# Performance work log

Hardware: AMD Instinct MI355X
Metric: run time of the kernel (lower is better)

## Reference

```python
import jax, jax.numpy as jnp
import numpy as np

BLANK_ID = 0


def setup_inputs() -> dict:
    key = jax.random.key(0)
    ks = jax.random.split(key, 8)
    B, T, H, V = 32, 1000, 640, 5000
    s = 0.02
    tn_output = jax.random.normal(ks[0], (B, T, H), dtype=jnp.float32)
    embed = jax.random.normal(ks[1], (V, H), dtype=jnp.float32) * s
    Wx = jax.random.normal(ks[2], (H, 4 * H), dtype=jnp.float32) * s  # LSTM input weights
    Wh = jax.random.normal(ks[3], (H, 4 * H), dtype=jnp.float32) * s  # LSTM recurrent weights
    b = jnp.zeros((4 * H,), dtype=jnp.float32)
    Wc = jax.random.normal(ks[4], (H, V), dtype=jnp.float32) * s     # classifier weights
    bc = jnp.zeros((V,), dtype=jnp.float32)
    return {"tn_output": tn_output, "embed": embed, "Wx": Wx, "Wh": Wh,
            "b": b, "Wc": Wc, "bc": bc}


def _lstm_step(tok, h, c, embed, Wx, Wh, b):
    # tok: [B] int32, h/c: [B,H]
    x = embed[tok]                                   # [B,H] gather (PN embedding)
    g = x @ Wx + h @ Wh + b                          # [B,4H]
    i, f, gg, o = jnp.split(g, 4, axis=-1)
    c2 = jax.nn.sigmoid(f) * c + jax.nn.sigmoid(i) * jnp.tanh(gg)
    h2 = jax.nn.sigmoid(o) * jnp.tanh(c2)
    return h2, c2


def reference(tn_output, embed, Wx, Wh, b, Wc, bc):
    """Batched transducer greedy decode (beam_size=1 path).
    Per t: joint = tanh(TN_t + out_PN); logits = joint @ Wc + bc; log_softmax;
    argmax; if != blank, emit token, accumulate logp, advance PN state (masked).
    Returns (logp_scores [B], predictions [B,T] with blank where no emission).
    """
    B, T, H = tn_output.shape
    tok0 = jnp.full((B,), BLANK_ID, dtype=jnp.int32)
    h0 = jnp.zeros((B, H), dtype=tn_output.dtype)
    c0 = jnp.zeros((B, H), dtype=tn_output.dtype)
    # initial PN forward on the blank token (hidden = None -> zeros)
    h, c = _lstm_step(tok0, h0, c0, embed, Wx, Wh, b)
    out_PN = h

    def step(carry, tn_t):
        h, c, out_PN, tok, scores = carry
        logits = jnp.tanh(tn_t + out_PN) @ Wc + bc            # joint ('sum') + classifier
        logp = jax.nn.log_softmax(logits, axis=-1)            # [B,V]
        pos = jnp.argmax(logp, axis=-1)                       # [B]
        val = jnp.max(logp, axis=-1)                          # [B]
        upd = pos != BLANK_ID
        scores = scores + jnp.where(upd, val, 0.0)
        new_tok = jnp.where(upd, pos.astype(jnp.int32), tok)
        h2, c2 = _lstm_step(new_tok, h, c, embed, Wx, Wh, b)
        m = upd[:, None]
        h = jnp.where(m, h2, h)
        c = jnp.where(m, c2, c)
        out_PN = jnp.where(m, h2, out_PN)
        emit = jnp.where(upd, pos, BLANK_ID).astype(jnp.int32)
        return (h, c, out_PN, new_tok, scores), emit

    carry0 = (h, c, out_PN, tok0, jnp.zeros((B,), dtype=tn_output.dtype))
    (h, c, out_PN, tok, scores), emits = jax.lax.scan(
        step, carry0, jnp.swapaxes(tn_output, 0, 1))          # scan over time
    preds = jnp.swapaxes(emits, 0, 1)                          # [B,T]
    return scores, preds
```

## Files before the change

### kernel.cpp

```cpp
#include <hip/hip_runtime.h>
#include <float.h>

#define BB 32
#define TT 1000
#define HH 640
#define H4 2560
#define VV 5000
#define NLOG 157
#define NGATE 80
#define NB   240

#define O_JOINT 0
#define O_HT    20480
#define O_PM    40960
#define O_PS    46080
#define O_PI    51200
#define O_BAR   56320
#define O_CT    56960
#define O_PNT   77440
#define O_XWXB  97920
#define XWXB_ELEMS ((size_t)VV * (size_t)H4)
#define O_WHP   (O_XWXB + 12800000)
#define WHP_ELEMS ((size_t)NGATE * HH * 32)

typedef unsigned int u32;
typedef unsigned long long u64;
typedef float vf4 __attribute__((ext_vector_type(4)));

__device__ __forceinline__ float sigf(float x) { return 1.0f / (1.0f + expf(-x)); }

__device__ __forceinline__ float ldc1(const float* p) {
  u32 v = __hip_atomic_load((const u32*)p, __ATOMIC_RELAXED, __HIP_MEMORY_SCOPE_AGENT);
  return __uint_as_float(v);
}
__device__ __forceinline__ void stc1(float* p, float x) {
  __hip_atomic_store((u32*)p, __float_as_uint(x), __ATOMIC_RELAXED, __HIP_MEMORY_SCOPE_AGENT);
}

__device__ __forceinline__ void stage_sc1_full(float* dst, const float* src, int tid) {
  const float* p0 = src + 4 * (tid + 0 * 512);
  const float* p1 = src + 4 * (tid + 1 * 512);
  const float* p2 = src + 4 * (tid + 2 * 512);
  const float* p3 = src + 4 * (tid + 3 * 512);
  const float* p4 = src + 4 * (tid + 4 * 512);
  const float* p5 = src + 4 * (tid + 5 * 512);
  const float* p6 = src + 4 * (tid + 6 * 512);
  const float* p7 = src + 4 * (tid + 7 * 512);
  const float* p8 = src + 4 * (tid + 8 * 512);
  const float* p9 = src + 4 * (tid + 9 * 512);
  float4 a0, a1, a2, a3, a4, a5, a6, a7, a8, a9;
  asm volatile(
      "global_load_dwordx4 %0, %10, off sc0 sc1\n\t"
      "global_load_dwordx4 %1, %11, off sc0 sc1\n\t"
      "global_load_dwordx4 %2, %12, off sc0 sc1\n\t"
      "global_load_dwordx4 %3, %13, off sc0 sc1\n\t"
      "global_load_dwordx4 %4, %14, off sc0 sc1\n\t"
      "global_load_dwordx4 %5, %15, off sc0 sc1\n\t"
      "global_load_dwordx4 %6, %16, off sc0 sc1\n\t"
      "global_load_dwordx4 %7, %17, off sc0 sc1\n\t"
      "global_load_dwordx4 %8, %18, off sc0 sc1\n\t"
      "global_load_dwordx4 %9, %19, off sc0 sc1\n\t"
      "s_waitcnt vmcnt(0)"
      : "=&v"(a0), "=&v"(a1), "=&v"(a2), "=&v"(a3), "=&v"(a4),
        "=&v"(a5), "=&v"(a6), "=&v"(a7), "=&v"(a8), "=&v"(a9)
      : "v"(p0), "v"(p1), "v"(p2), "v"(p3), "v"(p4),
        "v"(p5), "v"(p6), "v"(p7), "v"(p8), "v"(p9)
      : "memory");
  float4* d4 = (float4*)dst;
  d4[tid + 0 * 512] = a0;
  d4[tid + 1 * 512] = a1;
  d4[tid + 2 * 512] = a2;
  d4[tid + 3 * 512] = a3;
  d4[tid + 4 * 512] = a4;
  d4[tid + 5 * 512] = a5;
  d4[tid + 6 * 512] = a6;
  d4[tid + 7 * 512] = a7;
  d4[tid + 8 * 512] = a8;
  d4[tid + 9 * 512] = a9;
}

__device__ __forceinline__ void grid_bar(unsigned* bar, unsigned epoch) {
  __syncthreads();
  if (threadIdx.x == 0) {
    const int g = (int)blockIdx.x / 30;
    unsigned* cnt = bar + g * 32;
    unsigned* gen = bar + (9 + g) * 32;
    asm volatile("s_waitcnt vmcnt(0)" ::: "memory");
    unsigned a = __hip_atomic_fetch_add(cnt, 1u, __ATOMIC_RELAXED, __HIP_MEMORY_SCOPE_AGENT);
    if (a == 30u * epoch - 1u) {
      unsigned* root = bar + 8 * 32;
      unsigned r = __hip_atomic_fetch_add(root, 1u, __ATOMIC_RELAXED, __HIP_MEMORY_SCOPE_AGENT);
      if (r == 8u * epoch - 1u) {
#pragma unroll
        for (int i = 0; i < 8; ++i)
          __hip_atomic_store(bar + (9 + i) * 32, epoch, __ATOMIC_RELAXED, __HIP_MEMORY_SCOPE_AGENT);
      }
    }
    while (__hip_atomic_load(gen, __ATOMIC_RELAXED, __HIP_MEMORY_SCOPE_AGENT) < epoch)
      __builtin_amdgcn_s_sleep(1);
  }
  __syncthreads();
}

__global__ __launch_bounds__(256) void precompute_k(const float* __restrict__ embed,
                                                    const float* __restrict__ Wx,
                                                    const float* __restrict__ bias,
                                                    float* __restrict__ xwxb) {
  __shared__ float embT[HH * 17];
  const int tid = threadIdx.x;
  const int v0 = blockIdx.y * 16;
  const int c0 = blockIdx.x * 256 + (tid & 63) * 4;
  const int vg = tid >> 6;
  for (int i = tid; i < 16 * 160; i += 256) {
    int vr = i / 160, kq = i - vr * 160;
    int v = v0 + vr; if (v >= VV) v = VV - 1;
    float4 e = *(const float4*)&embed[(size_t)v * HH + kq * 4];
    embT[(kq * 4 + 0) * 17 + vr] = e.x;
    embT[(kq * 4 + 1) * 17 + vr] = e.y;
    embT[(kq * 4 + 2) * 17 + vr] = e.z;
    embT[(kq * 4 + 3) * 17 + vr] = e.w;
  }
  __syncthreads();
  float acc[16];
#pragma unroll
  for (int i = 0; i < 16; ++i) acc[i] = 0.f;
#pragma unroll 4
  for (int k = 0; k < HH; ++k) {
    float4 wv = *(const float4*)&Wx[(size_t)k * H4 + c0];
#pragma unroll
    for (int i = 0; i < 4; ++i) {
      float e = embT[k * 17 + vg * 4 + i];
      acc[i * 4 + 0] += e * wv.x;
      acc[i * 4 + 1] += e * wv.y;
      acc[i * 4 + 2] += e * wv.z;
      acc[i * 4 + 3] += e * wv.w;
    }
  }
  float4 bv = *(const float4*)&bias[c0];
#pragma unroll
  for (int i = 0; i < 4; ++i) {
    int v = v0 + vg * 4 + i;
    if (v < VV) {
      float4 r;
      r.x = acc[i * 4 + 0] + bv.x; r.y = acc[i * 4 + 1] + bv.y;
      r.z = acc[i * 4 + 2] + bv.z; r.w = acc[i * 4 + 3] + bv.w;
      *(float4*)&xwxb[(size_t)v * H4 + c0] = r;
    }
  }
}

__global__ __launch_bounds__(256) void repack_k(const float* __restrict__ Wh,
                                                float* __restrict__ whp) {
  const int q = blockIdx.x;
  for (int i = threadIdx.x; i < HH * 32; i += 256) {
    int k = i >> 5, lc = i & 31;
    whp[((size_t)q * HH + k) * 32 + lc] =
        Wh[(size_t)k * H4 + (lc >> 3) * HH + q * 8 + (lc & 7)];
  }
}

__global__ __launch_bounds__(256) void init_k(const float* __restrict__ tn,
                                              const float* __restrict__ embed,
                                              const float* __restrict__ Wx,
                                              const float* __restrict__ bias,
                                              float* ws, int use_table) {
  const int tid = threadIdx.x, bid = blockIdx.x;
  const int b = tid & 31, c8 = tid >> 5;
  const int j = bid * 8 + c8;
  if (bid == 0) {
    unsigned* bar = (unsigned*)(ws + O_BAR);
    for (int i = tid; i < 17 * 32; i += 256) bar[i] = 0u;
  }
  const float* xwxb = ws + O_XWXB;
  float g4[4];
  if (use_table) {
#pragma unroll
    for (int g = 0; g < 4; ++g) g4[g] = xwxb[g * HH + j];
  } else {
#pragma unroll
    for (int g = 0; g < 4; ++g) g4[g] = bias[g * HH + j];
#pragma unroll 4
    for (int k = 0; k < HH; ++k) {
      float xv = embed[k];
#pragma unroll
      for (int g = 0; g < 4; ++g) g4[g] += xv * Wx[(size_t)k * H4 + g * HH + j];
    }
  }
  float c1 = sigf(g4[0]) * tanhf(g4[2]);
  float h1 = sigf(g4[3]) * tanhf(c1);
  ws[O_CT + j * 32 + b] = c1;
  ws[O_HT + j * 32 + b] = h1;
  ws[O_PNT + j * 32 + b] = h1;
  ws[O_JOINT + j * 32 + b] = tanhf(tn[(size_t)b * TT * HH + j] + h1);
}

__global__ __launch_bounds__(512) void decode_k(const float* __restrict__ tn,
                                                const float* __restrict__ embed,
                                                const float* __restrict__ Wx,
                                                const float* __restrict__ bias,
                                                const float* __restrict__ Wh,
                                                const float* __restrict__ Wc,
                                                const float* __restrict__ bc,
                                                float* __restrict__ out,
                                                float* ws, int use_table, int use_pack) {
  __shared__ float joint_s[20480];
  __shared__ float smem[10800];
  __shared__ float hwh_s[1056];
  __shared__ float c_s[256];
  __shared__ float pn_s[256];
  __shared__ int s_tok[32];
  __shared__ int s_upd[32];
  __shared__ int s_ptok[32];
  __shared__ float s_scores[32];
  const int tid = threadIdx.x, bid = blockIdx.x;
  unsigned* bar = (unsigned*)(ws + O_BAR);
  const float* xwxb = ws + O_XWXB;
  const bool is_log = (bid < NLOG);
  const bool is_gate = (bid >= NLOG) && (bid < NLOG + NGATE);
  const int q = bid - NLOG;

  if (tid < 32) { s_ptok[tid] = 0; s_scores[tid] = 0.f; }
  if (is_gate && tid < 256) {
    const int jj = tid >> 5, b = tid & 31;
    c_s[jj * 32 + b] = ws[O_CT + (q * 8 + jj) * 32 + b];
    pn_s[jj * 32 + b] = ws[O_PNT + (q * 8 + jj) * 32 + b];
  }
  __syncthreads();

  const int lane = tid & 63, wvv = tid >> 6;
  const int sub = lane >> 5;
  const int cg  = lane & 3;
  const int bg  = (lane >> 2) & 7;
  const int kb  = (wvv * 2 + sub) * 40;
  const float* wbase;
  int wstride;
  if (is_log) {
    int c = bid * 32 + cg * 8;
    if (c > VV - 8) c = VV - 8;
    wbase = Wc + (size_t)kb * VV + c;
    wstride = VV;
  } else if (use_pack) {
    wbase = ws + O_WHP + ((size_t)q * HH + kb) * 32 + cg * 8;
    wstride = 32;
  } else {
    wbase = Wh + (size_t)kb * H4 + cg * HH + q * 8;
    wstride = H4;
  }
  const float* jb0 = joint_s + kb * 32 + bg * 4;

  unsigned epoch = 0;
  for (int t = 0; t < TT; ++t) {
    float tnv = 0.f;

    if (is_log || is_gate) {
      if (is_gate && tid < 256 && t + 1 < TT)
        tnv = tn[((size_t)(tid & 31) * TT + (t + 1)) * HH + q * 8 + (tid >> 5)];
      stage_sc1_full(joint_s, ws + (is_log ? O_JOINT : O_HT), tid);
      __syncthreads();

      float acc[32];
#pragma unroll
      for (int i = 0; i < 32; ++i) acc[i] = 0.f;
      if (is_log) {
        const float* wp = wbase;
        const float* jp = jb0;
#pragma unroll 4
        for (int kk = 0; kk < 40; ++kk) {
          float4 w0 = *(const float4*)(wp);
          float4 w1 = *(const float4*)(wp + 4);
          float4 jv = *(const float4*)(jp);
          wp += wstride;
          jp += 32;
          acc[0]  += w0.x * jv.x; acc[1]  += w0.x * jv.y; acc[2]  += w0.x * jv.z; acc[3]  += w0.x * jv.w;
          acc[4]  += w0.y * jv.x; acc[5]  += w0.y * jv.y; acc[6]  += w0.y * jv.z; acc[7]  += w0.y * jv.w;
          acc[8]  += w0.z * jv.x; acc[9]  += w0.z * jv.y; acc[10] += w0.z * jv.z; acc[11] += w0.z * jv.w;
          acc[12] += w0.w * jv.x; acc[13] += w0.w * jv.y; acc[14] += w0.w * jv.z; acc[15] += w0.w * jv.w;
          acc[16] += w1.x * jv.x; acc[17] += w1.x * jv.y; acc[18] += w1.x * jv.z; acc[19] += w1.x * jv.w;
          acc[20] += w1.y * jv.x; acc[21] += w1.y * jv.y; acc[22] += w1.y * jv.z; acc[23] += w1.y * jv.w;
          acc[24] += w1.z * jv.x; acc[25] += w1.z * jv.y; acc[26] += w1.z * jv.z; acc[27] += w1.z * jv.w;
          acc[28] += w1.w * jv.x; acc[29] += w1.w * jv.y; acc[30] += w1.w * jv.z; acc[31] += w1.w * jv.w;
        }
      } else {
        const float* wp = wbase;
        const float* jp = jb0;
#pragma unroll 4
        for (int kk = 0; kk < 40; ++kk) {
          vf4 w0 = __builtin_nontemporal_load((const vf4*)(wp));
          vf4 w1 = __builtin_nontemporal_load((const vf4*)(wp + 4));
          float4 jv = *(const float4*)(jp);
          wp += wstride;
          jp += 32;
          acc[0]  += w0.x * jv.x; acc[1]  += w0.x * jv.y; acc[2]  += w0.x * jv.z; acc[3]  += w0.x * jv.w;
          acc[4]  += w0.y * jv.x; acc[5]  += w0.y * jv.y; acc[6]  += w0.y * jv.z; acc[7]  += w0.y * jv.w;
          acc[8]  += w0.z * jv.x; acc[9]  += w0.z * jv.y; acc[10] += w0.z * jv.z; acc[11] += w0.z * jv.w;
          acc[12] += w0.w * jv.x; acc[13] += w0.w * jv.y; acc[14] += w0.w * jv.z; acc[15] += w0.w * jv.w;
          acc[16] += w1.x * jv.x; acc[17] += w1.x * jv.y; acc[18] += w1.x * jv.z; acc[19] += w1.x * jv.w;
          acc[20] += w1.y * jv.x; acc[21] += w1.y * jv.y; acc[22] += w1.y * jv.z; acc[23] += w1.y * jv.w;
          acc[24] += w1.z * jv.x; acc[25] += w1.z * jv.y; acc[26] += w1.z * jv.z; acc[27] += w1.z * jv.w;
          acc[28] += w1.w * jv.x; acc[29] += w1.w * jv.y; acc[30] += w1.w * jv.z; acc[31] += w1.w * jv.w;
        }
      }
#pragma unroll
      for (int i = 0; i < 32; ++i) acc[i] += __shfl_xor(acc[i], 32);
      float* part = smem;
      if (sub == 0) {
        float* pb = part + wvv * 1152 + bg * 4;
#pragma unroll
        for (int c = 0; c < 8; ++c)
          *(float4*)&pb[(cg * 8 + c) * 36] =
              make_float4(acc[c * 4 + 0], acc[c * 4 + 1], acc[c * 4 + 2], acc[c * 4 + 3]);
      }
      __syncthreads();

      const int b = tid & 31, colg = tid >> 5;
      if (is_log) {
        float* lm = smem + 9216;
        float* lsv = smem + 9744;
        int* lix = (int*)(smem + 10272);
        float m = -FLT_MAX; int ix = 0;
        float lv[2];
#pragma unroll
        for (int i = 0; i < 2; ++i) {
          const int cl = colg * 2 + i;
          float s = 0.f;
#pragma unroll
          for (int qq = 0; qq < 8; ++qq) s += part[qq * 1152 + cl * 36 + b];
          int cgl = bid * 32 + cl;
          float l = (cgl < VV) ? s + bc[cgl] : -FLT_MAX;
          lv[i] = l;
          if (l > m) { m = l; ix = cgl; }
        }
        float e = 0.f;
        if (m > -FLT_MAX) {
#pragma unroll
          for (int i = 0; i < 2; ++i) e += expf(lv[i] - m);
        }
        lm[colg * 33 + b] = m; lsv[colg * 33 + b] = e; lix[colg * 33 + b] = ix;
        __syncthreads();
        if (tid < 32) {
          float m2 = lm[tid], s2 = lsv[tid]; int ix2 = lix[tid];
#pragma unroll
          for (int qq = 1; qq < 16; ++qq) {
            float M = lm[qq * 33 + tid], S = lsv[qq * 33 + tid]; int I = lix[qq * 33 + tid];
            if (M > m2) { s2 = s2 * expf(m2 - M) + S; m2 = M; ix2 = I; }
            else if (M > -FLT_MAX) { s2 += S * expf(M - m2); }
          }
          stc1(&ws[O_PM + bid * 32 + tid], m2);
          stc1(&ws[O_PS + bid * 32 + tid], s2);
          stc1(&ws[O_PI + bid * 32 + tid], __int_as_float(ix2));
        }
      } else {
#pragma unroll
        for (int i = 0; i < 2; ++i) {
          const int cl = colg * 2 + i;
          float s = 0.f;
#pragma unroll
          for (int qq = 0; qq < 8; ++qq) s += part[qq * 1152 + cl * 36 + b];
          hwh_s[cl * 33 + b] = s;
        }
      }
    }
    epoch++;
    grid_bar(bar, epoch);

    if (is_gate) {
      float* rm = smem;
      float* rs = smem + 528;
      int* ri = (int*)(smem + 1056);
      float* gmat = smem + 1584;
      float* xl = smem + 2640;
      const int r = tid & 31, c16 = tid >> 5;
      {
        float Ms[10], Ss[10]; int Is[10];
#pragma unroll
        for (int i = 0; i < 10; ++i) {
          int idx = c16 * 10 + i;
          bool v = (idx < NLOG);
          int ic = v ? idx : 0;
          Ms[i] = ldc1(&ws[O_PM + ic * 32 + r]);
          Ss[i] = ldc1(&ws[O_PS + ic * 32 + r]);
          Is[i] = __float_as_int(ldc1(&ws[O_PI + ic * 32 + r]));
          if (!v) { Ms[i] = -FLT_MAX; Ss[i] = 0.f; Is[i] = 0; }
        }
        float m = -FLT_MAX, s = 0.f; int ix = 0;
#pragma unroll
        for (int i = 0; i < 10; ++i) {
          if (Ms[i] > m) { s = s * expf(m - Ms[i]) + Ss[i]; m = Ms[i]; ix = Is[i]; }
          else if (Ms[i] > -FLT_MAX) { s += Ss[i] * expf(Ms[i] - m); }
        }
        rm[c16 * 33 + r] = m; rs[c16 * 33 + r] = s; ri[c16 * 33 + r] = ix;
      }
      __syncthreads();
      if (tid < 32) {
        float m = rm[tid], s = rs[tid]; int ix = ri[tid];
#pragma unroll
        for (int qq = 1; qq < 16; ++qq) {
          float M = rm[qq * 33 + tid], S = rs[qq * 33 + tid]; int I = ri[qq * 33 + tid];
          if (M > m) { s = s * expf(m - M) + S; m = M; ix = I; }
          else { s += S * expf(M - m); }
        }
        int pos = ix;
        int upd = (pos != 0) ? 1 : 0;
        int ntk = upd ? pos : s_ptok[tid];
        s_tok[tid] = ntk; s_upd[tid] = upd; s_ptok[tid] = ntk;
        if (bid == NLOG) {
          float sc = s_scores[tid];
          if (upd) sc -= logf(s);
          s_scores[tid] = sc;
          out[BB + (size_t)tid * TT + t] = upd ? (float)pos : 0.0f;
          if (t == TT - 1) out[tid] = sc;
        }
      }
      __syncthreads();

      const int b = tid & 31;
      float gv[2];
#pragma unroll
      for (int h = 0; h < 2; ++h) {
        int lc = (tid >> 5) + h * 16;
        int wcol = (lc >> 3) * HH + q * 8 + (lc & 7);
        float v = hwh_s[lc * 33 + b];
        if (use_table) v += __builtin_nontemporal_load(&xwxb[(size_t)s_tok[b] * H4 + wcol]);
        else v += bias[wcol];
        gv[h] = v;
      }
      if (!use_table) {
        for (int st = 0; st < 4; ++st) {
          const int k0 = st * 160;
          __syncthreads();
          for (int i = tid; i < 32 * 160; i += 512) {
            int bb = i / 160, kk = i - bb * 160;
            xl[bb * 161 + kk] = embed[(size_t)s_tok[bb] * HH + k0 + kk];
          }
          __syncthreads();
          for (int k = 0; k < 160; ++k) {
            float xv = xl[b * 161 + k];
#pragma unroll
            for (int h = 0; h < 2; ++h) {
              int lc = (tid >> 5) + h * 16;
              int wcol = (lc >> 3) * HH + q * 8 + (lc & 7);
              gv[h] += xv * Wx[(size_t)(k0 + k) * H4 + wcol];
            }
          }
        }
      }
#pragma unroll
      for (int h = 0; h < 2; ++h) {
        int lc = (tid >> 5) + h * 16;
        gmat[lc * 33 + b] = gv[h];
      }
      __syncthreads();
      if (tid < 256) {
        const int jj = tid >> 5, b2 = tid & 31;
        float gi = gmat[(0 * 8 + jj) * 33 + b2];
        float gf = gmat[(1 * 8 + jj) * 33 + b2];
        float gg = gmat[(2 * 8 + jj) * 33 + b2];
        float go = gmat[(3 * 8 + jj) * 33 + b2];
        float cold = c_s[jj * 32 + b2];
        float c2 = sigf(gf) * cold + sigf(gi) * tanhf(gg);
        float h2 = sigf(go) * tanhf(c2);
        float pv;
        if (s_upd[b2]) {
          c_s[jj * 32 + b2] = c2;
          pn_s[jj * 32 + b2] = h2;
          stc1(&ws[O_HT + (q * 8 + jj) * 32 + b2], h2);
          pv = h2;
        } else {
          pv = pn_s[jj * 32 + b2];
        }
        if (t + 1 < TT)
          stc1(&ws[O_JOINT + (q * 8 + jj) * 32 + b2], tanhf(tnv + pv));
      }
    }
    epoch++;
    grid_bar(bar, epoch);
  }
}

extern "C" void kernel_launch(void* const* d_in, const int* in_sizes, int n_in,
                              void* d_out, int out_size, void* d_ws, size_t ws_size,
                              hipStream_t stream) {
  const float* tn    = (const float*)d_in[0];
  const float* embed = (const float*)d_in[1];
  const float* Wx    = (const float*)d_in[2];
  const float* Wh    = (const float*)d_in[3];
  const float* bias  = (const float*)d_in[4];
  const float* Wc    = (const float*)d_in[5];
  const float* bc    = (const float*)d_in[6];
  float* out = (float*)d_out;
  float* ws  = (float*)d_ws;

  const size_t need_table = (size_t)(O_XWXB + XWXB_ELEMS) * sizeof(float);
  const size_t need_pack  = (size_t)(O_WHP + WHP_ELEMS) * sizeof(float);
  const int use_table = (ws_size >= need_table) ? 1 : 0;
  const int use_pack  = (ws_size >= need_pack) ? 1 : 0;

  if (use_table)
    hipLaunchKernelGGL(precompute_k, dim3(10, 313), dim3(256), 0, stream,
                       embed, Wx, bias, ws + O_XWXB);
  if (use_pack)
    hipLaunchKernelGGL(repack_k, dim3(NGATE), dim3(256), 0, stream, Wh, ws + O_WHP);
  hipLaunchKernelGGL(init_k, dim3(80), dim3(256), 0, stream, tn, embed, Wx, bias, ws, use_table);
  hipLaunchKernelGGL(decode_k, dim3(NB), dim3(512), 0, stream,
                     tn, embed, Wx, bias, Wh, Wc, bc, out, ws, use_table, use_pack);
}
```

Baseline: 19.06 ms.

## Replace two grid barriers per step with point-to-point flag synchronization

Removes the hierarchical grid-wide barrier that ran twice per timestep. Logit blocks now publish a per-block progress flag, and gate blocks publish their own flag plus increment a counter once they have staged the previous hidden state. Gate blocks wait only on the flags they depend on, and the extra blocks exit early. This is meant to cut barrier latency and let the logit and gate phases overlap, at the cost of spin polling across many flags and more subtle memory-ordering requirements.

After: 30.97 ms. +62.5%, slower.

```diff
diff --git a/kernel.cpp b/kernel.cpp
--- a/kernel.cpp
+++ b/kernel.cpp
@@ -35,6 +35,12 @@
 }
 __device__ __forceinline__ void stc1(float* p, float x) {
   __hip_atomic_store((u32*)p, __float_as_uint(x), __ATOMIC_RELAXED, __HIP_MEMORY_SCOPE_AGENT);
+}
+__device__ __forceinline__ u32 ldu(const u32* p) {
+  return __hip_atomic_load(p, __ATOMIC_RELAXED, __HIP_MEMORY_SCOPE_AGENT);
+}
+__device__ __forceinline__ void stu(u32* p, u32 v) {
+  __hip_atomic_store(p, v, __ATOMIC_RELAXED, __HIP_MEMORY_SCOPE_AGENT);
 }
 
 __device__ __forceinline__ void stage_sc1_full(float* dst, const float* src, int tid) {
@@ -79,29 +85,6 @@
   d4[tid + 9 * 512] = a9;
 }
 
-__device__ __forceinline__ void grid_bar(unsigned* bar, unsigned epoch) {
-  __syncthreads();
-  if (threadIdx.x == 0) {
-    const int g = (int)blockIdx.x / 30;
-    unsigned* cnt = bar + g * 32;
-    unsigned* gen = bar + (9 + g) * 32;
-    asm volatile("s_waitcnt vmcnt(0)" ::: "memory");
-    unsigned a = __hip_atomic_fetch_add(cnt, 1u, __ATOMIC_RELAXED, __HIP_MEMORY_SCOPE_AGENT);
-    if (a == 30u * epoch - 1u) {
-      unsigned* root = bar + 8 * 32;
-      unsigned r = __hip_atomic_fetch_add(root, 1u, __ATOMIC_RELAXED, __HIP_MEMORY_SCOPE_AGENT);
-      if (r == 8u * epoch - 1u) {
-#pragma unroll
-        for (int i = 0; i < 8; ++i)
-          __hip_atomic_store(bar + (9 + i) * 32, epoch, __ATOMIC_RELAXED, __HIP_MEMORY_SCOPE_AGENT);
-      }
-    }
-    while (__hip_atomic_load(gen, __ATOMIC_RELAXED, __HIP_MEMORY_SCOPE_AGENT) < epoch)
-      __builtin_amdgcn_s_sleep(1);
-  }
-  __syncthreads();
-}
-
 __global__ __launch_bounds__(256) void precompute_k(const float* __restrict__ embed,
                                                     const float* __restrict__ Wx,
                                                     const float* __restrict__ bias,
@@ -168,7 +151,7 @@
   const int b = tid & 31, c8 = tid >> 5;
   const int j = bid * 8 + c8;
   if (bid == 0) {
-    unsigned* bar = (unsigned*)(ws + O_BAR);
+    u32* bar = (u32*)(ws + O_BAR);
     for (int i = tid; i < 17 * 32; i += 256) bar[i] = 0u;
   }
   const float* xwxb = ws + O_XWXB;
@@ -213,10 +196,14 @@
   __shared__ int s_ptok[32];
   __shared__ float s_scores[32];
   const int tid = threadIdx.x, bid = blockIdx.x;
-  unsigned* bar = (unsigned*)(ws + O_BAR);
-  const float* xwxb = ws + O_XWXB;
   const bool is_log = (bid < NLOG);
   const bool is_gate = (bid >= NLOG) && (bid < NLOG + NGATE);
+  if (!is_log && !is_gate) return;
+
+  u32* F1  = (u32*)(ws + O_BAR);
+  u32* F2  = (u32*)(ws + O_BAR) + 192;
+  u32* CRD = (u32*)(ws + O_BAR) + 288;
+  const float* xwxb = ws + O_XWXB;
   const int q = bid - NLOG;
 
   if (tid < 32) { s_ptok[tid] = 0; s_scores[tid] = 0.f; }
@@ -248,232 +235,249 @@
   }
   const float* jb0 = joint_s + kb * 32 + bg * 4;
 
-  unsigned epoch = 0;
   for (int t = 0; t < TT; ++t) {
+    if (tid < NGATE) {
+      while (ldu(F2 + tid) < (u32)t) __builtin_amdgcn_s_sleep(1);
+    }
+    __syncthreads();
+
     float tnv = 0.f;
-
-    if (is_log || is_gate) {
-      if (is_gate && tid < 256 && t + 1 < TT)
-        tnv = tn[((size_t)(tid & 31) * TT + (t + 1)) * HH + q * 8 + (tid >> 5)];
-      stage_sc1_full(joint_s, ws + (is_log ? O_JOINT : O_HT), tid);
+    if (is_gate && tid < 256 && t + 1 < TT)
+      tnv = tn[((size_t)(tid & 31) * TT + (t + 1)) * HH + q * 8 + (tid >> 5)];
+
+    stage_sc1_full(joint_s, ws + (is_log ? O_JOINT : O_HT), tid);
+    __syncthreads();
+    if (is_gate && tid == 0)
+      (void)__hip_atomic_fetch_add(CRD, 1u, __ATOMIC_RELAXED, __HIP_MEMORY_SCOPE_AGENT);
+
+    float acc[32];
+#pragma unroll
+    for (int i = 0; i < 32; ++i) acc[i] = 0.f;
+    if (is_log) {
+      const float* wp = wbase;
+      const float* jp = jb0;
+#pragma unroll 4
+      for (int kk = 0; kk < 40; ++kk) {
+        float4 w0 = *(const float4*)(wp);
+        float4 w1 = *(const float4*)(wp + 4);
+        float4 jv = *(const float4*)(jp);
+        wp += wstride;
+        jp += 32;
+        acc[0]  += w0.x * jv.x; acc[1]  += w0.x * jv.y; acc[2]  += w0.x * jv.z; acc[3]  += w0.x * jv.w;
+        acc[4]  += w0.y * jv.x; acc[5]  += w0.y * jv.y; acc[6]  += w0.y * jv.z; acc[7]  += w0.y * jv.w;
+        acc[8]  += w0.z * jv.x; acc[9]  += w0.z * jv.y; acc[10] += w0.z * jv.z; acc[11] += w0.z * jv.w;
+        acc[12] += w0.w * jv.x; acc[13] += w0.w * jv.y; acc[14] += w0.w * jv.z; acc[15] += w0.w * jv.w;
+        acc[16] += w1.x * jv.x; acc[17] += w1.x * jv.y; acc[18] += w1.x * jv.z; acc[19] += w1.x * jv.w;
+        acc[20] += w1.y * jv.x; acc[21] += w1.y * jv.y; acc[22] += w1.y * jv.z; acc[23] += w1.y * jv.w;
+        acc[24] += w1.z * jv.x; acc[25] += w1.z * jv.y; acc[26] += w1.z * jv.z; acc[27] += w1.z * jv.w;
+        acc[28] += w1.w * jv.x; acc[29] += w1.w * jv.y; acc[30] += w1.w * jv.z; acc[31] += w1.w * jv.w;
+      }
+    } else {
+      const float* wp = wbase;
+      const float* jp = jb0;
+#pragma unroll 4
+      for (int kk = 0; kk < 40; ++kk) {
+        vf4 w0 = __builtin_nontemporal_load((const vf4*)(wp));
+        vf4 w1 = __builtin_nontemporal_load((const vf4*)(wp + 4));
+        float4 jv = *(const float4*)(jp);
+        wp += wstride;
+        jp += 32;
+        acc[0]  += w0.x * jv.x; acc[1]  += w0.x * jv.y; acc[2]  += w0.x * jv.z; acc[3]  += w0.x * jv.w;
+        acc[4]  += w0.y * jv.x; acc[5]  += w0.y * jv.y; acc[6]  += w0.y * jv.z; acc[7]  += w0.y * jv.w;
+        acc[8]  += w0.z * jv.x; acc[9]  += w0.z * jv.y; acc[10] += w0.z * jv.z; acc[11] += w0.z * jv.w;
+        acc[12] += w0.w * jv.x; acc[13] += w0.w * jv.y; acc[14] += w0.w * jv.z; acc[15] += w0.w * jv.w;
+        acc[16] += w1.x * jv.x; acc[17] += w1.x * jv.y; acc[18] += w1.x * jv.z; acc[19] += w1.x * jv.w;
+        acc[20] += w1.y * jv.x; acc[21] += w1.y * jv.y; acc[22] += w1.y * jv.z; acc[23] += w1.y * jv.w;
+        acc[24] += w1.z * jv.x; acc[25] += w1.z * jv.y; acc[26] += w1.z * jv.z; acc[27] += w1.z * jv.w;
+        acc[28] += w1.w * jv.x; acc[29] += w1.w * jv.y; acc[30] += w1.w * jv.z; acc[31] += w1.w * jv.w;
+      }
+    }
+#pragma unroll
+    for (int i = 0; i < 32; ++i) acc[i] += __shfl_xor(acc[i], 32);
+    float* part = smem;
+    if (sub == 0) {
+      float* pb = part + wvv * 1152 + bg * 4;
+#pragma unroll
+      for (int c = 0; c < 8; ++c)
+        *(float4*)&pb[(cg * 8 + c) * 36] =
+            make_float4(acc[c * 4 + 0], acc[c * 4 + 1], acc[c * 4 + 2], acc[c * 4 + 3]);
+    }
+    __syncthreads();
+
+    const int b = tid & 31, colg = tid >> 5;
+    if (is_log) {
+      float* lm = smem + 9216;
+      float* lsv = smem + 9744;
+      int* lix = (int*)(smem + 10272);
+      float m = -FLT_MAX; int ix = 0;
+      float lv[2];
+#pragma unroll
+      for (int i = 0; i < 2; ++i) {
+        const int cl = colg * 2 + i;
+        float s = 0.f;
+#pragma unroll
+        for (int qq = 0; qq < 8; ++qq) s += part[qq * 1152 + cl * 36 + b];
+        int cgl = bid * 32 + cl;
+        float l = (cgl < VV) ? s + bc[cgl] : -FLT_MAX;
+        lv[i] = l;
+        if (l > m) { m = l; ix = cgl; }
+      }
+      float e = 0.f;
+      if (m > -FLT_MAX) {
+#pragma unroll
+        for (int i = 0; i < 2; ++i) e += expf(lv[i] - m);
+      }
+      lm[colg * 33 + b] = m; lsv[colg * 33 + b] = e; lix[colg * 33 + b] = ix;
       __syncthreads();
-
-      float acc[32];
-#pragma unroll
-      for (int i = 0; i < 32; ++i) acc[i] = 0.f;
-      if (is_log) {
-        const float* wp = wbase;
-        const float* jp = jb0;
-#pragma unroll 4
-        for (int kk = 0; kk < 40; ++kk) {
-          float4 w0 = *(const float4*)(wp);
-          float4 w1 = *(const float4*)(wp + 4);
-          float4 jv = *(const float4*)(jp);
-          wp += wstride;
-          jp += 32;
-          acc[0]  += w0.x * jv.x; acc[1]  += w0.x * jv.y; acc[2]  += w0.x * jv.z; acc[3]  += w0.x * jv.w;
-          acc[4]  += w0.y * jv.x; acc[5]  += w0.y * jv.y; acc[6]  += w0.y * jv.z; acc[7]  += w0.y * jv.w;
-          acc[8]  += w0.z * jv.x; acc[9]  += w0.z * jv.y; acc[10] += w0.z * jv.z; acc[11] += w0.z * jv.w;
-          acc[12] += w0.w * jv.x; acc[13] += w0.w * jv.y; acc[14] += w0.w * jv.z; acc[15] += w0.w * jv.w;
-          acc[16] += w1.x * jv.x; acc[17] += w1.x * jv.y; acc[18] += w1.x * jv.z; acc[19] += w1.x * jv.w;
-          acc[20] += w1.y * jv.x; acc[21] += w1.y * jv.y; acc[22] += w1.y * jv.z; acc[23] += w1.y * jv.w;
-          acc[24] += w1.z * jv.x; acc[25] += w1.z * jv.y; acc[26] += w1.z * jv.z; acc[27] += w1.z * jv.w;
-          acc[28] += w1.w * jv.x; acc[29] += w1.w * jv.y; acc[30] += w1.w * jv.z; acc[31] += w1.w * jv.w;
+      if (tid < 32) {
+        float m2 = lm[tid], s2 = lsv[tid]; int ix2 = lix[tid];
+#pragma unroll
+        for (int qq = 1; qq < 16; ++qq) {
+          float M = lm[qq * 33 + tid], S = lsv[qq * 33 + tid]; int I = lix[qq * 33 + tid];
+          if (M > m2) { s2 = s2 * expf(m2 - M) + S; m2 = M; ix2 = I; }
+          else if (M > -FLT_MAX) { s2 += S * expf(M - m2); }
         }
-      } else {
-        const float* wp = wbase;
-        const float* jp = jb0;
-#pragma unroll 4
-        for (int kk = 0; kk < 40; ++kk) {
-          vf4 w0 = __builtin_nontemporal_load((const vf4*)(wp));
-          vf4 w1 = __builtin_nontemporal_load((const vf4*)(wp + 4));
-          float4 jv = *(const float4*)(jp);
-          wp += wstride;
-          jp += 32;
-          acc[0]  += w0.x * jv.x; acc[1]  += w0.x * jv.y; acc[2]  += w0.x * jv.z; acc[3]  += w0.x * jv.w;
-          acc[4]  += w0.y * jv.x; acc[5]  += w0.y * jv.y; acc[6]  += w0.y * jv.z; acc[7]  += w0.y * jv.w;
-          acc[8]  += w0.z * jv.x; acc[9]  += w0.z * jv.y; acc[10] += w0.z * jv.z; acc[11] += w0.z * jv.w;
-          acc[12] += w0.w * jv.x; acc[13] += w0.w * jv.y; acc[14] += w0.w * jv.z; acc[15] += w0.w * jv.w;
-          acc[16] += w1.x * jv.x; acc[17] += w1.x * jv.y; acc[18] += w1.x * jv.z; acc[19] += w1.x * jv.w;
-          acc[20] += w1.y * jv.x; acc[21] += w1.y * jv.y; acc[22] += w1.y * jv.z; acc[23] += w1.y * jv.w;
-          acc[24] += w1.z * jv.x; acc[25] += w1.z * jv.y; acc[26] += w1.z * jv.z; acc[27] += w1.z * jv.w;
-          acc[28] += w1.w * jv.x; acc[29] += w1.w * jv.y; acc[30] += w1.w * jv.z; acc[31] += w1.w * jv.w;
-        }
-      }
-#pragma unroll
-      for (int i = 0; i < 32; ++i) acc[i] += __shfl_xor(acc[i], 32);
-      float* part = smem;
-      if (sub == 0) {
-        float* pb = part + wvv * 1152 + bg * 4;
-#pragma unroll
-        for (int c = 0; c < 8; ++c)
-          *(float4*)&pb[(cg * 8 + c) * 36] =
-              make_float4(acc[c * 4 + 0], acc[c * 4 + 1], acc[c * 4 + 2], acc[c * 4 + 3]);
+        stc1(&ws[O_PM + bid * 32 + tid], m2);
+        stc1(&ws[O_PS + bid * 32 + tid], s2);
+        stc1(&ws[O_PI + bid * 32 + tid], __int_as_float(ix2));
       }
       __syncthreads();
-
-      const int b = tid & 31, colg = tid >> 5;
-      if (is_log) {
-        float* lm = smem + 9216;
-        float* lsv = smem + 9744;
-        int* lix = (int*)(smem + 10272);
-        float m = -FLT_MAX; int ix = 0;
-        float lv[2];
-#pragma unroll
-        for (int i = 0; i < 2; ++i) {
-          const int cl = colg * 2 + i;
-          float s = 0.f;
-#pragma unroll
-          for (int qq = 0; qq < 8; ++qq) s += part[qq * 1152 + cl * 36 + b];
-          int cgl = bid * 32 + cl;
-          float l = (cgl < VV) ? s + bc[cgl] : -FLT_MAX;
-          lv[i] = l;
-          if (l > m) { m = l; ix = cgl; }
-        }
-        float e = 0.f;
-        if (m > -FLT_MAX) {
-#pragma unroll
-          for (int i = 0; i < 2; ++i) e += expf(lv[i] - m);
-        }
-        lm[colg * 33 + b] = m; lsv[colg * 33 + b] = e; lix[colg * 33 + b] = ix;
-        __syncthreads();
-        if (tid < 32) {
-          float m2 = lm[tid], s2 = lsv[tid]; int ix2 = lix[tid];
-#pragma unroll
-          for (int qq = 1; qq < 16; ++qq) {
-            float M = lm[qq * 33 + tid], S = lsv[qq * 33 + tid]; int I = lix[qq * 33 + tid];
-            if (M > m2) { s2 = s2 * expf(m2 - M) + S; m2 = M; ix2 = I; }
-            else if (M > -FLT_MAX) { s2 += S * expf(M - m2); }
-          }
-          stc1(&ws[O_PM + bid * 32 + tid], m2);
-          stc1(&ws[O_PS + bid * 32 + tid], s2);
-          stc1(&ws[O_PI + bid * 32 + tid], __int_as_float(ix2));
-        }
-      } else {
-#pragma unroll
-        for (int i = 0; i < 2; ++i) {
-          const int cl = colg * 2 + i;
-          float s = 0.f;
-#pragma unroll
-          for (int qq = 0; qq < 8; ++qq) s += part[qq * 1152 + cl * 36 + b];
-          hwh_s[cl * 33 + b] = s;
-        }
-      }
-    }
-    epoch++;
-    grid_bar(bar, epoch);
-
-    if (is_gate) {
-      float* rm = smem;
-      float* rs = smem + 528;
-      int* ri = (int*)(smem + 1056);
-      float* gmat = smem + 1584;
-      float* xl = smem + 2640;
-      const int r = tid & 31, c16 = tid >> 5;
-      {
-        float Ms[10], Ss[10]; int Is[10];
+      if (tid == 0) stu(F1 + bid, (u32)(t + 1));
+      continue;
+    }
+
+#pragma unroll
+    for (int i = 0; i < 2; ++i) {
+      const int cl = colg * 2 + i;
+      float s = 0.f;
+#pragma unroll
+      for (int qq = 0; qq < 8; ++qq) s += part[qq * 1152 + cl * 36 + b];
+      hwh_s[cl * 33 + b] = s;
+    }
+
+    __syncthreads();
+    float* rm = smem;
+    float* rs = smem + 528;
+    int* ri = (int*)(smem + 1056);
+    float* gmat = smem + 1584;
+    float* xl = smem + 2640;
+    const int r = tid & 31, c16 = tid >> 5;
+    {
+      for (;;) {
+        bool ok = true;
 #pragma unroll
         for (int i = 0; i < 10; ++i) {
           int idx = c16 * 10 + i;
-          bool v = (idx < NLOG);
-          int ic = v ? idx : 0;
-          Ms[i] = ldc1(&ws[O_PM + ic * 32 + r]);
-          Ss[i] = ldc1(&ws[O_PS + ic * 32 + r]);
-          Is[i] = __float_as_int(ldc1(&ws[O_PI + ic * 32 + r]));
-          if (!v) { Ms[i] = -FLT_MAX; Ss[i] = 0.f; Is[i] = 0; }
+          if (idx < NLOG && ldu(F1 + idx) < (u32)(t + 1)) ok = false;
         }
-        float m = -FLT_MAX, s = 0.f; int ix = 0;
-#pragma unroll
-        for (int i = 0; i < 10; ++i) {
-          if (Ms[i] > m) { s = s * expf(m - Ms[i]) + Ss[i]; m = Ms[i]; ix = Is[i]; }
-          else if (Ms[i] > -FLT_MAX) { s += Ss[i] * expf(Ms[i] - m); }
+        if (ok) break;
+        __builtin_amdgcn_s_sleep(1);
+      }
+      float Ms[10], Ss[10]; int Is[10];
+#pragma unroll
+      for (int i = 0; i < 10; ++i) {
+        int idx = c16 * 10 + i;
+        bool v = (idx < NLOG);
+        int ic = v ? idx : 0;
+        Ms[i] = ldc1(&ws[O_PM + ic * 32 + r]);
+        Ss[i] = ldc1(&ws[O_PS + ic * 32 + r]);
+        Is[i] = __float_as_int(ldc1(&ws[O_PI + ic * 32 + r]));
+        if (!v) { Ms[i] = -FLT_MAX; Ss[i] = 0.f; Is[i] = 0; }
+      }
+      float m = -FLT_MAX, s = 0.f; int ix = 0;
+#pragma unroll
+      for (int i = 0; i < 10; ++i) {
+        if (Ms[i] > m) { s = s * expf(m - Ms[i]) + Ss[i]; m = Ms[i]; ix = Is[i]; }
+        else if (Ms[i] > -FLT_MAX) { s += Ss[i] * expf(Ms[i] - m); }
+      }
+      rm[c16 * 33 + r] = m; rs[c16 * 33 + r] = s; ri[c16 * 33 + r] = ix;
+    }
+    __syncthreads();
+    if (tid < 32) {
+      float m = rm[tid], s = rs[tid]; int ix = ri[tid];
+#pragma unroll
+      for (int qq = 1; qq < 16; ++qq) {
+        float M = rm[qq * 33 + tid], S = rs[qq * 33 + tid]; int I = ri[qq * 33 + tid];
+        if (M > m) { s = s * expf(m - M) + S; m = M; ix = I; }
+        else { s += S * expf(M - m); }
+      }
+      int pos = ix;
+      int upd = (pos != 0) ? 1 : 0;
+      int ntk = upd ? pos : s_ptok[tid];
+      s_tok[tid] = ntk; s_upd[tid] = upd; s_ptok[tid] = ntk;
+      if (bid == NLOG) {
+        float sc = s_scores[tid];
+        if (upd) sc -= logf(s);
+        s_scores[tid] = sc;
+        out[BB + (size_t)tid * TT + t] = upd ? (float)pos : 0.0f;
+        if (t == TT - 1) out[tid] = sc;
+      }
+    }
+    __syncthreads();
+
+    float gv[2];
+#pragma unroll
+    for (int h = 0; h < 2; ++h) {
+      int lc = (tid >> 5) + h * 16;
+      int wcol = (lc >> 3) * HH + q * 8 + (lc & 7);
+      float v = hwh_s[lc * 33 + b];
+      if (use_table) v += __builtin_nontemporal_load(&xwxb[(size_t)s_tok[b] * H4 + wcol]);
+      else v += bias[wcol];
+      gv[h] = v;
+    }
+    if (!use_table) {
+      for (int st = 0; st < 4; ++st) {
+        const int k0 = st * 160;
+        __syncthreads();
+        for (int i = tid; i < 32 * 160; i += 512) {
+          int bb = i / 160, kk = i - bb * 160;
+          xl[bb * 161 + kk] = embed[(size_t)s_tok[bb] * HH + k0 + kk];
         }
-        rm[c16 * 33 + r] = m; rs[c16 * 33 + r] = s; ri[c16 * 33 + r] = ix;
-      }
-      __syncthreads();
-      if (tid < 32) {
-        float m = rm[tid], s = rs[tid]; int ix = ri[tid];
-#pragma unroll
-        for (int qq = 1; qq < 16; ++qq) {
-          float M = rm[qq * 33 + tid], S = rs[qq * 33 + tid]; int I = ri[qq * 33 + tid];
-          if (M > m) { s = s * expf(m - M) + S; m = M; ix = I; }
-          else { s += S * expf(M - m); }
-        }
-        int pos = ix;
-        int upd = (pos != 0) ? 1 : 0;
-        int ntk = upd ? pos : s_ptok[tid];
-        s_tok[tid] = ntk; s_upd[tid] = upd; s_ptok[tid] = ntk;
-        if (bid == NLOG) {
-          float sc = s_scores[tid];
-          if (upd) sc -= logf(s);
-          s_scores[tid] = sc;
-          out[BB + (size_t)tid * TT + t] = upd ? (float)pos : 0.0f;
-          if (t == TT - 1) out[tid] = sc;
-        }
-      }
-      __syncthreads();
-
-      const int b = tid & 31;
-      float gv[2];
-#pragma unroll
-      for (int h = 0; h < 2; ++h) {
-        int lc = (tid >> 5) + h * 16;
-        int wcol = (lc >> 3) * HH + q * 8 + (lc & 7);
-        float v = hwh_s[lc * 33 + b];
-        if (use_table) v += __builtin_nontemporal_load(&xwxb[(size_t)s_tok[b] * H4 + wcol]);
-        else v += bias[wcol];
-        gv[h] = v;
-      }
-      if (!use_table) {
-        for (int st = 0; st < 4; ++st) {
-          const int k0 = st * 160;
-          __syncthreads();
-          for (int i = tid; i < 32 * 160; i += 512) {
-            int bb = i / 160, kk = i - bb * 160;
-            xl[bb * 161 + kk] = embed[(size_t)s_tok[bb] * HH + k0 + kk];
-          }
-          __syncthreads();
-          for (int k = 0; k < 160; ++k) {
-            float xv = xl[b * 161 + k];
-#pragma unroll
-            for (int h = 0; h < 2; ++h) {
-              int lc = (tid >> 5) + h * 16;
-              int wcol = (lc >> 3) * HH + q * 8 + (lc & 7);
-              gv[h] += xv * Wx[(size_t)(k0 + k) * H4 + wcol];
-            }
+        __syncthreads();
+        for (int k = 0; k < 160; ++k) {
+          float xv = xl[b * 161 + k];
+#pragma unroll
+          for (int h = 0; h < 2; ++h) {
+            int lc = (tid >> 5) + h * 16;
+            int wcol = (lc >> 3) * HH + q * 8 + (lc & 7);
+            gv[h] += xv * Wx[(size_t)(k0 + k) * H4 + wcol];
           }
         }
       }
-#pragma unroll
-      for (int h = 0; h < 2; ++h) {
-        int lc = (tid >> 5) + h * 16;
-        gmat[lc * 33 + b] = gv[h];
-      }
-      __syncthreads();
-      if (tid < 256) {
-        const int jj = tid >> 5, b2 = tid & 31;
-        float gi = gmat[(0 * 8 + jj) * 33 + b2];
-        float gf = gmat[(1 * 8 + jj) * 33 + b2];
-        float gg = gmat[(2 * 8 + jj) * 33 + b2];
-        float go = gmat[(3 * 8 + jj) * 33 + b2];
-        float cold = c_s[jj * 32 + b2];
-        float c2 = sigf(gf) * cold + sigf(gi) * tanhf(gg);
-        float h2 = sigf(go) * tanhf(c2);
-        float pv;
-        if (s_upd[b2]) {
-          c_s[jj * 32 + b2] = c2;
-          pn_s[jj * 32 + b2] = h2;
-          stc1(&ws[O_HT + (q * 8 + jj) * 32 + b2], h2);
-          pv = h2;
-        } else {
-          pv = pn_s[jj * 32 + b2];
-        }
-        if (t + 1 < TT)
-          stc1(&ws[O_JOINT + (q * 8 + jj) * 32 + b2], tanhf(tnv + pv));
-      }
-    }
-    epoch++;
-    grid_bar(bar, epoch);
+    }
+#pragma unroll
+    for (int h = 0; h < 2; ++h) {
+      int lc = (tid >> 5) + h * 16;
+      gmat[lc * 33 + b] = gv[h];
+    }
+    __syncthreads();
+    if (tid == 0) {
+      while (ldu(CRD) < 80u * (u32)(t + 1)) __builtin_amdgcn_s_sleep(1);
+    }
+    __syncthreads();
+    if (tid < 256) {
+      const int jj = tid >> 5, b2 = tid & 31;
+      float gi = gmat[(0 * 8 + jj) * 33 + b2];
+      float gf = gmat[(1 * 8 + jj) * 33 + b2];
+      float gg = gmat[(2 * 8 + jj) * 33 + b2];
+      float go = gmat[(3 * 8 + jj) * 33 + b2];
+      float cold = c_s[jj * 32 + b2];
+      float c2 = sigf(gf) * cold + sigf(gi) * tanhf(gg);
+      float h2 = sigf(go) * tanhf(c2);
+      float pv;
+      if (s_upd[b2]) {
+        c_s[jj * 32 + b2] = c2;
+        pn_s[jj * 32 + b2] = h2;
+        stc1(&ws[O_HT + (q * 8 + jj) * 32 + b2], h2);
+        pv = h2;
+      } else {
+        pv = pn_s[jj * 32 + b2];
+      }
+      if (t + 1 < TT)
+        stc1(&ws[O_JOINT + (q * 8 + jj) * 32 + b2], tanhf(tnv + pv));
+    }
+    __syncthreads();
+    if (tid == 0) stu(F2 + q, (u32)(t + 1));
   }
 }
 
```
